# Kernel optimization log

Hardware: AMD Instinct MI355X
Metric: run time of the kernel (lower is better)

The kernel has to match this reference:

```python
import jax, jax.numpy as jnp
import numpy as np
import math

NX = 1024
N_HEAD = 16
HEAD_DIM = NX // N_HEAD
N_CTX = 2048
REL_VOCAB = 64
B = 2
S = 2048


def setup_inputs() -> dict:
    key = jax.random.key(0)
    ks = jax.random.split(key, 7)
    x = jax.random.normal(ks[0], (B, S, NX), dtype=jnp.float32)
    rel = jax.random.randint(ks[1], (B, S, S), 0, REL_VOCAB, dtype=jnp.int64)
    sc = 0.02
    Wqkv = jax.random.normal(ks[2], (NX, 3 * NX), dtype=jnp.float32) * sc
    bqkv = jnp.zeros((3 * NX,), dtype=jnp.float32)
    Wproj = jax.random.normal(ks[3], (NX, NX), dtype=jnp.float32) * sc
    bproj = jnp.zeros((NX,), dtype=jnp.float32)
    rel_emb = jax.random.normal(ks[4], (REL_VOCAB, N_HEAD), dtype=jnp.float32) * sc
    return {"x": x, "Wqkv": Wqkv, "bqkv": bqkv, "Wproj": Wproj,
            "bproj": bproj, "rel_emb": rel_emb, "rel": rel}


def reference(x, Wqkv, bqkv, Wproj, bproj, rel_emb, rel):
    Bsz, Sq, _ = x.shape
    qkv = x @ Wqkv + bqkv                      # [B,S,3*nx]
    q, k, v = jnp.split(qkv, 3, axis=-1)
    def split_heads(t):                        # [B,S,nx] -> [B,H,S,D]
        return t.reshape(Bsz, Sq, N_HEAD, HEAD_DIM).transpose(0, 2, 1, 3)
    q, k, v = split_heads(q), split_heads(k), split_heads(v)
    w = jnp.einsum('bhqd,bhkd->bhqk', q, k) / math.sqrt(HEAD_DIM)
    bmask = jnp.tril(jnp.ones((Sq, Sq), dtype=w.dtype))[None, None]  # [1,1,S,S]
    w = w * bmask - 1e10 * (1.0 - bmask)
    relw = rel_emb[rel].transpose(0, 3, 1, 2)  # [B,S,S,H] -> [B,H,S,S]
    w = w * (relw * bmask)                     # faithful: masked scores become 0
    p = jax.nn.softmax(w, axis=-1)
    a = jnp.einsum('bhqk,bhkd->bhqd', p, v)
    a = a.transpose(0, 2, 1, 3).reshape(Bsz, Sq, NX)  # merge heads
    return a @ Wproj + bproj
```

## Files before the change

### kernel.cpp

```cpp
#include <hip/hip_runtime.h>

typedef unsigned short u16;
typedef unsigned char u8;
typedef __attribute__((ext_vector_type(8))) short short8;
typedef __attribute__((ext_vector_type(4))) float f32x4;

#define GLD16(g, l) __builtin_amdgcn_global_load_lds( \
    (const __attribute__((address_space(1))) void*)(g), \
    (__attribute__((address_space(3))) void*)(l), 16, 0, 0)

__device__ __forceinline__ float bf2f(u16 u){
  union { unsigned int i; float f; } v; v.i = ((unsigned int)u) << 16; return v.f;
}
__device__ __forceinline__ u16 f2bf(float f){
  union { float f; unsigned int i; } v; v.f = f;
  unsigned int u = v.i;
  unsigned int r = (u + 0x7FFFu + ((u >> 16) & 1u)) >> 16;
  return (u16)r;
}

__global__ void cvt_k(const float* __restrict__ x, u16* __restrict__ o, int n4){
  int i = blockIdx.x * 256 + threadIdx.x;
  if (i >= n4) return;
  float4 v = ((const float4*)x)[i];
  unsigned long long pk = (unsigned long long)f2bf(v.x)
    | ((unsigned long long)f2bf(v.y) << 16)
    | ((unsigned long long)f2bf(v.z) << 32)
    | ((unsigned long long)f2bf(v.w) << 48);
  ((unsigned long long*)o)[i] = pk;
}

__global__ void rel8_k(const int* __restrict__ r, u8* __restrict__ o, int n4){
  int i = blockIdx.x * 256 + threadIdx.x;
  if (i >= n4) return;
  int4 v = ((const int4*)r)[i];
  unsigned int pk = (unsigned int)(v.x & 255) | ((unsigned int)(v.y & 255) << 8)
    | ((unsigned int)(v.z & 255) << 16) | ((unsigned int)(v.w & 255) << 24);
  ((unsigned int*)o)[i] = pk;
}

__global__ void tconv_k(const float* __restrict__ W, u16* __restrict__ Wt, int K, int N){
  __shared__ float tl[32][33];
  int n0 = blockIdx.x * 32, k0 = blockIdx.y * 32;
  for (int i = threadIdx.y; i < 32; i += 8)
    tl[i][threadIdx.x] = W[(size_t)(k0 + i) * N + n0 + threadIdx.x];
  __syncthreads();
  for (int i = threadIdx.y; i < 32; i += 8)
    Wt[(size_t)(n0 + i) * K + k0 + threadIdx.x] = f2bf(tl[threadIdx.x][i]);
}

template<int MODE>
__global__ __launch_bounds__(256) void gemm_bt_k(const u16* __restrict__ A, const u16* __restrict__ Bt,
                                                 const float* __restrict__ bias,
                                                 u16* __restrict__ oq, u16* __restrict__ okk, u16* __restrict__ ov,
                                                 float* __restrict__ of,
                                                 int M, int N, int K){
  __shared__ u16 la[128 * 32];
  __shared__ u16 lb[128 * 32];
  const int t = threadIdx.x, w = t >> 6, lane = t & 63;
  const int l15 = lane & 15, l4 = lane >> 4;
  const int m0 = blockIdx.y * 128, n0 = blockIdx.x * 128;
  const int wr = w >> 1, wc = w & 1;
  f32x4 acc[4][4] = {};
  const u16* Abase = A + (size_t)m0 * K;
  const u16* Bbase = Bt + (size_t)n0 * K;
  for (int kt = 0; kt < K; kt += 32){
    __syncthreads();
#pragma unroll
    for (int i = 0; i < 2; ++i){
      int chunk = i * 256 + t;
      int row = chunk >> 2, cg = chunk & 3;
      GLD16(Abase + (size_t)row * K + kt + cg * 8, &la[(i * 256 + w * 64) * 8]);
    }
#pragma unroll
    for (int i = 0; i < 2; ++i){
      int chunk = i * 256 + t;
      int row = chunk >> 2, cg = chunk & 3;
      GLD16(Bbase + (size_t)row * K + kt + cg * 8, &lb[(i * 256 + w * 64) * 8]);
    }
    asm volatile("s_waitcnt vmcnt(0)" ::: "memory");
    __syncthreads();
    short8 af[4], bfr[4];
#pragma unroll
    for (int mi = 0; mi < 4; ++mi)
      af[mi] = *(const short8*)&la[(wr * 64 + mi * 16 + l15) * 32 + l4 * 8];
#pragma unroll
    for (int ni = 0; ni < 4; ++ni)
      bfr[ni] = *(const short8*)&lb[(wc * 64 + ni * 16 + l15) * 32 + l4 * 8];
#pragma unroll
    for (int mi = 0; mi < 4; ++mi)
#pragma unroll
      for (int ni = 0; ni < 4; ++ni)
        acc[mi][ni] = __builtin_amdgcn_mfma_f32_16x16x32_bf16(af[mi], bfr[ni], acc[mi][ni], 0, 0, 0);
  }
#pragma unroll
  for (int mi = 0; mi < 4; ++mi){
#pragma unroll
    for (int ni = 0; ni < 4; ++ni){
#pragma unroll
      for (int r = 0; r < 4; ++r){
        int m = m0 + wr * 64 + mi * 16 + l4 * 4 + r;
        int n = n0 + wc * 64 + ni * 16 + l15;
        float v = acc[mi][ni][r] + bias[n];
        if (MODE == 0){
          int tt = n >> 10, rr = n & 1023, head = rr >> 6, d = rr & 63;
          int b = m >> 11, s = m & 2047;
          u16* dst = (tt == 0) ? oq : (tt == 1) ? okk : ov;
          dst[(((size_t)(b * 16 + head)) * 2048 + s) * 64 + d] = f2bf(v);
        } else {
          of[(size_t)m * N + n] = v;
        }
      }
    }
  }
}

__global__ __launch_bounds__(256) void transpose_v_k(const u16* __restrict__ vb, u16* __restrict__ vt,
                                                     float* __restrict__ vpart){
  __shared__ u16 tl[64][65];
  int bh = blockIdx.x >> 5, c = blockIdx.x & 31, s0 = c * 64;
  int t = threadIdx.x;
#pragma unroll
  for (int rsub = 0; rsub < 16; ++rsub){
    int idx = rsub * 256 + t;
    int i = idx >> 6, d = idx & 63;
    tl[i][d] = vb[(((size_t)bh * 2048) + s0 + i) * 64 + d];
  }
  __syncthreads();
#pragma unroll
  for (int rsub = 0; rsub < 16; ++rsub){
    int idx = rsub * 256 + t;
    int d = idx >> 6, j = idx & 63;
    vt[(((size_t)bh * 64) + d) * 2048 + s0 + j] = tl[j][d];
  }
  if (t < 64){
    float s = 0.f;
#pragma unroll 8
    for (int j = 0; j < 64; ++j) s += bf2f(tl[j][t]);
    vpart[((size_t)bh * 32 + c) * 64 + t] = s;
  }
}

__global__ void vsufscan_k(const float* __restrict__ vpart, float* __restrict__ vsuf){
  int bh = blockIdx.x, d = threadIdx.x;
  float run = 0.f;
  vsuf[((size_t)bh * 33 + 32) * 64 + d] = 0.f;
  for (int c = 31; c >= 0; --c){
    run += vpart[((size_t)bh * 32 + c) * 64 + d];
    vsuf[((size_t)bh * 33 + c) * 64 + d] = run;
  }
}

template<int U8>
__global__ __launch_bounds__(256, 2) void attn_k(const u16* __restrict__ qb, const u16* __restrict__ kb,
                                                 const u16* __restrict__ vt, const float* __restrict__ vsuf,
                                                 const void* __restrict__ relp, const float* __restrict__ rel_emb,
                                                 u16* __restrict__ ab){
  __shared__ u16 Kt[2][64 * 64];
  __shared__ u16 Vt[2][64 * 64];
  __shared__ u16 Pl[4][16 * 64];
  __shared__ float remb[64];
  const int qp = blockIdx.x, bh = blockIdx.y;
  const int b = bh >> 4, h = bh & 15;
  const int TA = qp, TB = 31 - qp;
  const int q0A = TA * 64, q0B = TB * 64;
  const int t = threadIdx.x, w = t >> 6, lane = t & 63;
  const int l15 = lane & 15, l4 = lane >> 4;
  if (t < 64) remb[t] = rel_emb[t * 16 + h] * (0.125f * 1.44269504088896f);
  const u16* kbh = kb + ((size_t)bh * 2048) * 64;
  const u16* vbh = vt + ((size_t)bh * 64) * 2048;
  const u16* qA = qb + (((size_t)bh * 2048) + q0A + w * 16 + l15) * 64 + l4 * 8;
  const u16* qB = qb + (((size_t)bh * 2048) + q0B + w * 16 + l15) * 64 + l4 * 8;
  const short8 aqA0 = *(const short8*)qA, aqA1 = *(const short8*)(qA + 32);
  const short8 aqB0 = *(const short8*)qB, aqB1 = *(const short8*)(qB + 32);
  const size_t relA = ((size_t)b * 2048 + q0A + w * 16 + l4 * 4) * 2048;
  const size_t relB = ((size_t)b * 2048 + q0B + w * 16 + l4 * 4) * 2048;
  const u8* rel8 = (const u8*)relp;
  const int* rel32 = (const int*)relp;

  const int srow0 = (t >> 3), srow1 = 32 + (t >> 3);
  const int scs = t & 7;
  const int sc0 = scs ^ (srow0 & 7), sc1 = scs ^ (srow1 & 7);
  const int sldsoff = (w * 64) * 8;

#define STAGE(ktile, buf) do {                                                       \
    GLD16(kbh + (size_t)((ktile) * 64 + srow0) * 64 + sc0 * 8, &Kt[buf][sldsoff]);   \
    GLD16(kbh + (size_t)((ktile) * 64 + srow1) * 64 + sc1 * 8, &Kt[buf][2048 + sldsoff]); \
    GLD16(vbh + (size_t)srow0 * 2048 + (ktile) * 64 + sc0 * 8, &Vt[buf][sldsoff]);   \
    GLD16(vbh + (size_t)srow1 * 2048 + (ktile) * 64 + sc1 * 8, &Vt[buf][2048 + sldsoff]); \
  } while (0)

  f32x4 acc[4] = {};
  float rsum[4] = {0.f, 0.f, 0.f, 0.f};
  int relc[16], reln[16];

  STAGE(0, 0);
#pragma unroll
  for (int q = 0; q < 16; ++q){
    int ni = q >> 2, r = q & 3;
    size_t off = relA + (size_t)r * 2048 + ni * 16 + l15;
    relc[q] = U8 ? (int)rel8[off] : rel32[off];
  }
  __syncthreads();

  auto writeout = [&](int Td, int q0){
    const float* sufp = vsuf + ((size_t)bh * 33 + (Td + 1)) * 64;
    float suf[4];
#pragma unroll
    for (int ni = 0; ni < 4; ++ni) suf[ni] = sufp[ni * 16 + l15];
    float fn = (float)(2048 - (Td + 1) * 64);
#pragma unroll
    for (int r = 0; r < 4; ++r){
      float s = rsum[r];
      s += __shfl_xor(s, 1, 16);
      s += __shfl_xor(s, 2, 16);
      s += __shfl_xor(s, 4, 16);
      s += __shfl_xor(s, 8, 16);
      float invZ = 1.f / (s + fn);
      int qg = q0 + w * 16 + l4 * 4 + r;
#pragma unroll
      for (int ni = 0; ni < 4; ++ni){
        float o = (acc[ni][r] + suf[ni]) * invZ;
        ab[((size_t)b * 2048 + qg) * 1024 + h * 64 + ni * 16 + l15] = f2bf(o);
      }
    }
  };

  const int TOT = TA + TB + 2;
  for (int it = 0; it < TOT; ++it){
    const bool isA = (it <= TA);
    const int kt = isA ? it : (it - TA - 1);
    const int cur = it & 1;
    const int Tlim = isA ? TA : TB;

    if (it + 1 < TOT){
      const bool nIsA = (it + 1 <= TA);
      const int nkt = nIsA ? (it + 1) : (it - TA);
      STAGE(nkt, cur ^ 1);
      const size_t nrel = (nIsA ? relA : relB) + (size_t)nkt * 64;
#pragma unroll
      for (int q = 0; q < 16; ++q){
        int ni = q >> 2, r = q & 3;
        size_t off = nrel + (size_t)r * 2048 + ni * 16 + l15;
        reln[q] = U8 ? (int)rel8[off] : rel32[off];
      }
    }

    const short8 a0 = isA ? aqA0 : aqB0;
    const short8 a1 = isA ? aqA1 : aqB1;
    const bool diag = (kt == Tlim);

    float pr[4][4];
    __builtin_amdgcn_s_setprio(1);
#pragma unroll
    for (int ni = 0; ni < 4; ++ni){
      int krow = ni * 16 + l15;
      const u16* kbase = &Kt[cur][krow * 64];
      short8 bk0 = *(const short8*)&kbase[(l4 ^ (krow & 7)) * 8];
      short8 bk1 = *(const short8*)&kbase[((4 + l4) ^ (krow & 7)) * 8];
      f32x4 sf = {0.f, 0.f, 0.f, 0.f};
      sf = __builtin_amdgcn_mfma_f32_16x16x32_bf16(a0, bk0, sf, 0, 0, 0);
      sf = __builtin_amdgcn_mfma_f32_16x16x32_bf16(a1, bk1, sf, 0, 0, 0);
#pragma unroll
      for (int r = 0; r < 4; ++r){
        float sc = sf[r] * remb[relc[ni * 4 + r]];
        if (diag) sc = (krow <= w * 16 + l4 * 4 + r) ? sc : 0.f;
        float p = __builtin_amdgcn_exp2f(sc);
        rsum[r] += p;
        pr[ni][r] = p;
      }
    }
    __builtin_amdgcn_s_setprio(0);
#pragma unroll
    for (int ni = 0; ni < 4; ++ni)
#pragma unroll
      for (int r = 0; r < 4; ++r){
        int prow = l4 * 4 + r;
        int pcol = ni * 16 + l15;
        int pbyte = (prow * 128 + pcol * 2) ^ ((prow & 7) << 4);
        Pl[w][pbyte >> 1] = f2bf(pr[ni][r]);
      }
    asm volatile("s_waitcnt lgkmcnt(0)" ::: "memory");
    __builtin_amdgcn_sched_barrier(0);

    int byte0 = (l15 * 128 + l4 * 16) ^ ((l15 & 7) << 4);
    int byte1 = (l15 * 128 + 64 + l4 * 16) ^ ((l15 & 7) << 4);
    short8 pa0 = *(const short8*)&Pl[w][byte0 >> 1];
    short8 pa1 = *(const short8*)&Pl[w][byte1 >> 1];
    __builtin_amdgcn_s_setprio(1);
#pragma unroll
    for (int ni = 0; ni < 4; ++ni){
      int drow = ni * 16 + l15;
      const u16* vbase = &Vt[cur][drow * 64];
      short8 bv0 = *(const short8*)&vbase[(l4 ^ (drow & 7)) * 8];
      short8 bv1 = *(const short8*)&vbase[((4 + l4) ^ (drow & 7)) * 8];
      acc[ni] = __builtin_amdgcn_mfma_f32_16x16x32_bf16(pa0, bv0, acc[ni], 0, 0, 0);
      acc[ni] = __builtin_amdgcn_mfma_f32_16x16x32_bf16(pa1, bv1, acc[ni], 0, 0, 0);
    }
    __builtin_amdgcn_s_setprio(0);

    if (isA && it == TA){
      writeout(TA, q0A);
#pragma unroll
      for (int ni = 0; ni < 4; ++ni) acc[ni] = f32x4{0.f, 0.f, 0.f, 0.f};
#pragma unroll
      for (int r = 0; r < 4; ++r) rsum[r] = 0.f;
    }
#pragma unroll
    for (int q = 0; q < 16; ++q) relc[q] = reln[q];
    __syncthreads();
  }
#undef STAGE
  writeout(TB, q0B);
}

extern "C" void kernel_launch(void* const* d_in, const int* in_sizes, int n_in,
                              void* d_out, int out_size, void* d_ws, size_t ws_size,
                              hipStream_t stream){
  const float* x       = (const float*)d_in[0];
  const float* Wqkv    = (const float*)d_in[1];
  const float* bqkv    = (const float*)d_in[2];
  const float* Wproj   = (const float*)d_in[3];
  const float* bproj   = (const float*)d_in[4];
  const float* rel_emb = (const float*)d_in[5];
  const int*   rel     = (const int*)d_in[6];
  float* out = (float*)d_out;

  char* ws = (char*)d_ws;
  u16* xb     = (u16*)(ws);
  u16* wqkvT  = (u16*)(ws + (8ull  << 20));
  u16* wprojT = (u16*)(ws + (14ull << 20));
  u16* qb     = (u16*)(ws + (16ull << 20));
  u16* kb     = (u16*)(ws + (24ull << 20));
  u16* vb     = (u16*)(ws + (32ull << 20));
  u16* vtb    = (u16*)(ws + (40ull << 20));
  float* vsuf = (float*)(ws + (48ull << 20));
  float* vpart= (float*)(ws + (48ull << 20) + (512ull << 10));
  u8*   rel8  = (u8*)(ws + (49ull << 20));
  const bool useU8 = ws_size >= (58ull << 20);

  cvt_k<<<4096, 256, 0, stream>>>(x, xb, 1048576);
  tconv_k<<<dim3(96, 32), dim3(32, 8), 0, stream>>>(Wqkv, wqkvT, 1024, 3072);
  tconv_k<<<dim3(32, 32), dim3(32, 8), 0, stream>>>(Wproj, wprojT, 1024, 1024);
  if (useU8) rel8_k<<<8192, 256, 0, stream>>>(rel, rel8, 2097152);
  gemm_bt_k<0><<<dim3(24, 32), 256, 0, stream>>>(xb, wqkvT, bqkv, qb, kb, vb, nullptr, 4096, 3072, 1024);
  transpose_v_k<<<1024, 256, 0, stream>>>(vb, vtb, vpart);
  vsufscan_k<<<32, 64, 0, stream>>>(vpart, vsuf);
  if (useU8)
    attn_k<1><<<dim3(16, 32), 256, 0, stream>>>(qb, kb, vtb, vsuf, rel8, rel_emb, xb);
  else
    attn_k<0><<<dim3(16, 32), 256, 0, stream>>>(qb, kb, vtb, vsuf, rel, rel_emb, xb);
  gemm_bt_k<1><<<dim3(8, 32), 256, 0, stream>>>(xb, wprojT, bproj, nullptr, nullptr, nullptr, out, 4096, 1024, 1024);
}
```

Baseline: 169.7 us.

## Keep P in registers by transposing QK^T MFMA and permuting V layout

```diff
diff --git a/kernel.cpp b/kernel.cpp
--- a/kernel.cpp
+++ b/kernel.cpp
@@ -3,6 +3,7 @@
 typedef unsigned short u16;
 typedef unsigned char u8;
 typedef __attribute__((ext_vector_type(8))) short short8;
+typedef __attribute__((ext_vector_type(4))) short short4v;
 typedef __attribute__((ext_vector_type(4))) float f32x4;
 
 #define GLD16(g, l) __builtin_amdgcn_global_load_lds( \
@@ -17,6 +18,15 @@
   unsigned int u = v.i;
   unsigned int r = (u + 0x7FFFu + ((u >> 16) & 1u)) >> 16;
   return (u16)r;
+}
+
+__device__ __forceinline__ f32x4 mfma16(short4v a, short4v b, f32x4 c){
+#if __has_builtin(__builtin_amdgcn_mfma_f32_16x16x16bf16_1k)
+  return __builtin_amdgcn_mfma_f32_16x16x16bf16_1k(a, b, c, 0, 0, 0);
+#else
+  asm volatile("s_nop 1\n\tv_mfma_f32_16x16x16_bf16 %0, %1, %2, %0" : "+v"(c) : "v"(a), "v"(b));
+  return c;
+#endif
 }
 
 __global__ void cvt_k(const float* __restrict__ x, u16* __restrict__ o, int n4){
@@ -131,7 +141,8 @@
   for (int rsub = 0; rsub < 16; ++rsub){
     int idx = rsub * 256 + t;
     int d = idx >> 6, j = idx & 63;
-    vt[(((size_t)bh * 64) + d) * 2048 + s0 + j] = tl[j][d];
+    int pj = (j & 3) | (((j >> 2) & 3) << 4) | (((j >> 4) & 3) << 2);
+    vt[(((size_t)bh * 64) + d) * 2048 + s0 + pj] = tl[j][d];
   }
   if (t < 64){
     float s = 0.f;
@@ -158,28 +169,27 @@
                                                  u16* __restrict__ ab){
   __shared__ u16 Kt[2][64 * 64];
   __shared__ u16 Vt[2][64 * 64];
-  __shared__ u16 Pl[4][16 * 64];
   __shared__ float remb[64];
   const int qp = blockIdx.x, bh = blockIdx.y;
   const int b = bh >> 4, h = bh & 15;
   const int TA = qp, TB = 31 - qp;
   const int q0A = TA * 64, q0B = TB * 64;
-  const int t = threadIdx.x, w = t >> 6, lane = t & 63;
+  const int tid = threadIdx.x, w = tid >> 6, lane = tid & 63;
   const int l15 = lane & 15, l4 = lane >> 4;
-  if (t < 64) remb[t] = rel_emb[t * 16 + h] * (0.125f * 1.44269504088896f);
+  if (tid < 64) remb[tid] = rel_emb[tid * 16 + h] * (0.125f * 1.44269504088896f);
   const u16* kbh = kb + ((size_t)bh * 2048) * 64;
   const u16* vbh = vt + ((size_t)bh * 64) * 2048;
   const u16* qA = qb + (((size_t)bh * 2048) + q0A + w * 16 + l15) * 64 + l4 * 8;
   const u16* qB = qb + (((size_t)bh * 2048) + q0B + w * 16 + l15) * 64 + l4 * 8;
   const short8 aqA0 = *(const short8*)qA, aqA1 = *(const short8*)(qA + 32);
   const short8 aqB0 = *(const short8*)qB, aqB1 = *(const short8*)(qB + 32);
-  const size_t relA = ((size_t)b * 2048 + q0A + w * 16 + l4 * 4) * 2048;
-  const size_t relB = ((size_t)b * 2048 + q0B + w * 16 + l4 * 4) * 2048;
-  const u8* rel8 = (const u8*)relp;
-  const int* rel32 = (const int*)relp;
-
-  const int srow0 = (t >> 3), srow1 = 32 + (t >> 3);
-  const int scs = t & 7;
+  const u8*  r8A  = (const u8*)relp + ((size_t)b * 2048 + q0A + w * 16 + l15) * 2048;
+  const u8*  r8B  = (const u8*)relp + ((size_t)b * 2048 + q0B + w * 16 + l15) * 2048;
+  const int* r32A = (const int*)relp + ((size_t)b * 2048 + q0A + w * 16 + l15) * 2048;
+  const int* r32B = (const int*)relp + ((size_t)b * 2048 + q0B + w * 16 + l15) * 2048;
+
+  const int srow0 = (tid >> 3), srow1 = 32 + (tid >> 3);
+  const int scs = tid & 7;
   const int sc0 = scs ^ (srow0 & 7), sc1 = scs ^ (srow1 & 7);
   const int sldsoff = (w * 64) * 8;
 
@@ -191,40 +201,49 @@
   } while (0)
 
   f32x4 acc[4] = {};
-  float rsum[4] = {0.f, 0.f, 0.f, 0.f};
-  int relc[16], reln[16];
+  float rsum = 0.f;
+  unsigned int relc[4], reln[4];
+
+  auto relload = [&](bool isA, int kt, unsigned int* dst){
+    int off = kt * 64 + 4 * l4;
+    if (U8){
+      const u8* p = isA ? r8A : r8B;
+#pragma unroll
+      for (int t = 0; t < 4; ++t) dst[t] = *(const unsigned int*)(p + off + 16 * t);
+    } else {
+      const int* p = isA ? r32A : r32B;
+#pragma unroll
+      for (int t = 0; t < 4; ++t){
+        int4 v4 = *(const int4*)(p + off + 16 * t);
+        dst[t] = (unsigned int)(v4.x & 255) | ((unsigned int)(v4.y & 255) << 8)
+               | ((unsigned int)(v4.z & 255) << 16) | ((unsigned int)(v4.w & 255) << 24);
+      }
+    }
+  };
+
+  auto writeout = [&](int Td, int q0){
+    asm volatile("s_nop 7\n\ts_nop 7" :::);
+    float s = rsum;
+    s += __shfl_xor(s, 16);
+    s += __shfl_xor(s, 32);
+    float invZ = 1.f / (s + (float)(2048 - (Td + 1) * 64));
+    int qg = q0 + w * 16 + l15;
+    const float* sufp = vsuf + ((size_t)bh * 33 + Td + 1) * 64;
+#pragma unroll
+    for (int ni = 0; ni < 4; ++ni){
+      float4 sv = *(const float4*)(sufp + ni * 16 + 4 * l4);
+      unsigned int lo = (unsigned int)f2bf((acc[ni][0] + sv.x) * invZ)
+                      | ((unsigned int)f2bf((acc[ni][1] + sv.y) * invZ) << 16);
+      unsigned int hi = (unsigned int)f2bf((acc[ni][2] + sv.z) * invZ)
+                      | ((unsigned int)f2bf((acc[ni][3] + sv.w) * invZ) << 16);
+      uint2 o; o.x = lo; o.y = hi;
+      *(uint2*)(ab + ((size_t)b * 2048 + qg) * 1024 + h * 64 + ni * 16 + 4 * l4) = o;
+    }
+  };
 
   STAGE(0, 0);
-#pragma unroll
-  for (int q = 0; q < 16; ++q){
-    int ni = q >> 2, r = q & 3;
-    size_t off = relA + (size_t)r * 2048 + ni * 16 + l15;
-    relc[q] = U8 ? (int)rel8[off] : rel32[off];
-  }
+  relload(true, 0, relc);
   __syncthreads();
-
-  auto writeout = [&](int Td, int q0){
-    const float* sufp = vsuf + ((size_t)bh * 33 + (Td + 1)) * 64;
-    float suf[4];
-#pragma unroll
-    for (int ni = 0; ni < 4; ++ni) suf[ni] = sufp[ni * 16 + l15];
-    float fn = (float)(2048 - (Td + 1) * 64);
-#pragma unroll
-    for (int r = 0; r < 4; ++r){
-      float s = rsum[r];
-      s += __shfl_xor(s, 1, 16);
-      s += __shfl_xor(s, 2, 16);
-      s += __shfl_xor(s, 4, 16);
-      s += __shfl_xor(s, 8, 16);
-      float invZ = 1.f / (s + fn);
-      int qg = q0 + w * 16 + l4 * 4 + r;
-#pragma unroll
-      for (int ni = 0; ni < 4; ++ni){
-        float o = (acc[ni][r] + suf[ni]) * invZ;
-        ab[((size_t)b * 2048 + qg) * 1024 + h * 64 + ni * 16 + l15] = f2bf(o);
-      }
-    }
-  };
 
   const int TOT = TA + TB + 2;
   for (int it = 0; it < TOT; ++it){
@@ -237,65 +256,50 @@
       const bool nIsA = (it + 1 <= TA);
       const int nkt = nIsA ? (it + 1) : (it - TA);
       STAGE(nkt, cur ^ 1);
-      const size_t nrel = (nIsA ? relA : relB) + (size_t)nkt * 64;
-#pragma unroll
-      for (int q = 0; q < 16; ++q){
-        int ni = q >> 2, r = q & 3;
-        size_t off = nrel + (size_t)r * 2048 + ni * 16 + l15;
-        reln[q] = U8 ? (int)rel8[off] : rel32[off];
-      }
+      relload(nIsA, nkt, reln);
     }
 
     const short8 a0 = isA ? aqA0 : aqB0;
     const short8 a1 = isA ? aqA1 : aqB1;
     const bool diag = (kt == Tlim);
 
-    float pr[4][4];
+    short4v pk[4];
     __builtin_amdgcn_s_setprio(1);
 #pragma unroll
-    for (int ni = 0; ni < 4; ++ni){
-      int krow = ni * 16 + l15;
+    for (int t = 0; t < 4; ++t){
+      const int krow = 16 * t + l15;
       const u16* kbase = &Kt[cur][krow * 64];
-      short8 bk0 = *(const short8*)&kbase[(l4 ^ (krow & 7)) * 8];
+      short8 bk0 = *(const short8*)&kbase[((l4)     ^ (krow & 7)) * 8];
       short8 bk1 = *(const short8*)&kbase[((4 + l4) ^ (krow & 7)) * 8];
       f32x4 sf = {0.f, 0.f, 0.f, 0.f};
-      sf = __builtin_amdgcn_mfma_f32_16x16x32_bf16(a0, bk0, sf, 0, 0, 0);
-      sf = __builtin_amdgcn_mfma_f32_16x16x32_bf16(a1, bk1, sf, 0, 0, 0);
+      sf = __builtin_amdgcn_mfma_f32_16x16x32_bf16(bk0, a0, sf, 0, 0, 0);
+      sf = __builtin_amdgcn_mfma_f32_16x16x32_bf16(bk1, a1, sf, 0, 0, 0);
+      unsigned int rw = relc[t];
+      const int kk = 16 * t + 4 * l4;
 #pragma unroll
       for (int r = 0; r < 4; ++r){
-        float sc = sf[r] * remb[relc[ni * 4 + r]];
-        if (diag) sc = (krow <= w * 16 + l4 * 4 + r) ? sc : 0.f;
+        float sc = sf[r] * remb[(rw >> (8 * r)) & 255];
+        if (diag) sc = (kk + r <= w * 16 + l15) ? sc : 0.f;
         float p = __builtin_amdgcn_exp2f(sc);
-        rsum[r] += p;
-        pr[ni][r] = p;
+        rsum += p;
+        pk[t][r] = (short)f2bf(p);
       }
     }
-    __builtin_amdgcn_s_setprio(0);
-#pragma unroll
-    for (int ni = 0; ni < 4; ++ni)
-#pragma unroll
-      for (int r = 0; r < 4; ++r){
-        int prow = l4 * 4 + r;
-        int pcol = ni * 16 + l15;
-        int pbyte = (prow * 128 + pcol * 2) ^ ((prow & 7) << 4);
-        Pl[w][pbyte >> 1] = f2bf(pr[ni][r]);
-      }
-    asm volatile("s_waitcnt lgkmcnt(0)" ::: "memory");
-    __builtin_amdgcn_sched_barrier(0);
-
-    int byte0 = (l15 * 128 + l4 * 16) ^ ((l15 & 7) << 4);
-    int byte1 = (l15 * 128 + 64 + l4 * 16) ^ ((l15 & 7) << 4);
-    short8 pa0 = *(const short8*)&Pl[w][byte0 >> 1];
-    short8 pa1 = *(const short8*)&Pl[w][byte1 >> 1];
-    __builtin_amdgcn_s_setprio(1);
+    asm volatile("s_nop 2" :::);
 #pragma unroll
     for (int ni = 0; ni < 4; ++ni){
-      int drow = ni * 16 + l15;
+      const int drow = ni * 16 + l15;
       const u16* vbase = &Vt[cur][drow * 64];
-      short8 bv0 = *(const short8*)&vbase[(l4 ^ (drow & 7)) * 8];
-      short8 bv1 = *(const short8*)&vbase[((4 + l4) ^ (drow & 7)) * 8];
-      acc[ni] = __builtin_amdgcn_mfma_f32_16x16x32_bf16(pa0, bv0, acc[ni], 0, 0, 0);
-      acc[ni] = __builtin_amdgcn_mfma_f32_16x16x32_bf16(pa1, bv1, acc[ni], 0, 0, 0);
+      short8 vv0 = *(const short8*)&vbase[(((2 * l4)     ^ (drow & 7))) * 8];
+      short8 vv1 = *(const short8*)&vbase[(((2 * l4 + 1) ^ (drow & 7))) * 8];
+      short4v va0 = {vv0[0], vv0[1], vv0[2], vv0[3]};
+      short4v va1 = {vv0[4], vv0[5], vv0[6], vv0[7]};
+      short4v va2 = {vv1[0], vv1[1], vv1[2], vv1[3]};
+      short4v va3 = {vv1[4], vv1[5], vv1[6], vv1[7]};
+      acc[ni] = mfma16(va0, pk[0], acc[ni]);
+      acc[ni] = mfma16(va1, pk[1], acc[ni]);
+      acc[ni] = mfma16(va2, pk[2], acc[ni]);
+      acc[ni] = mfma16(va3, pk[3], acc[ni]);
     }
     __builtin_amdgcn_s_setprio(0);
 
@@ -303,11 +307,10 @@
       writeout(TA, q0A);
 #pragma unroll
       for (int ni = 0; ni < 4; ++ni) acc[ni] = f32x4{0.f, 0.f, 0.f, 0.f};
-#pragma unroll
-      for (int r = 0; r < 4; ++r) rsum[r] = 0.f;
-    }
-#pragma unroll
-    for (int q = 0; q < 16; ++q) relc[q] = reln[q];
+      rsum = 0.f;
+    }
+#pragma unroll
+    for (int t = 0; t < 4; ++t) relc[t] = reln[t];
     __syncthreads();
   }
 #undef STAGE
```

After: 172.8 us. About the same (+1.8%).
